# Kernel tuning notes

Hardware: AMD Instinct MI355X
Metric: run time of the kernel (lower is better)

## Reference

```python
import jax, jax.numpy as jnp
import numpy as np

DIM_MODEL = 1024
NUM_HEADS = 16
DROPOUT_P = 0.5
SCALE = float(np.sqrt(DIM_MODEL // NUM_HEADS))  # NOTE: source MULTIPLIES by this (unusual but faithful)
DROP_KEY = jax.random.key(42)


def setup_inputs() -> dict:
    key = jax.random.key(0)
    ks = jax.random.split(key, 9)
    B, LQ, LK, D = 4, 2048, 2048, DIM_MODEL
    s = 1.0 / np.sqrt(D)
    return {
        "query": jax.random.normal(ks[0], (B, LQ, D), jnp.float32),
        "key": jax.random.normal(ks[1], (B, LK, D), jnp.float32),
        "value": jax.random.normal(ks[2], (B, LK, D), jnp.float32),
        "Wq": jax.random.normal(ks[3], (D, D), jnp.float32) * s,
        "bq": jax.random.normal(ks[4], (D,), jnp.float32) * s,
        "Wk": jax.random.normal(ks[5], (D, D), jnp.float32) * s,
        "bk": jax.random.normal(ks[6], (D,), jnp.float32) * s,
        "Wv": jax.random.normal(ks[7], (D, D), jnp.float32) * s,
        "bv": jax.random.normal(ks[8], (D,), jnp.float32) * s,
    }


def reference(query, key, value, Wq, bq, Wk, bk, Wv, bv):
    # Linear projections (W stored as [in, out])
    q = jnp.einsum('bqd,de->bqe', query, Wq) + bq
    k = jnp.einsum('bkd,de->bke', key, Wk) + bk
    v = jnp.einsum('bkd,de->bke', value, Wv) + bv
    # scores scaled by MULTIPLYING sqrt(d_head), per source
    scores = jnp.einsum('bqe,bke->bqk', q, k) * SCALE
    probs = jax.nn.softmax(scores, axis=-1)
    # dropout (train mode, p=0.5), deterministic fixed key for reproducibility
    keep = jax.random.bernoulli(DROP_KEY, 1.0 - DROPOUT_P, probs.shape)
    probs = jnp.where(keep, probs / (1.0 - DROPOUT_P), 0.0)
    return jnp.einsum('bqk,bke->bqe', probs, v)
```

## Files before the change

kernel.cpp:

```cpp
#include <hip/hip_runtime.h>
#include <math.h>

#define BATCH  4
#define LSEQ   2048
#define DMODEL 1024
#define MROWS  (BATCH * LSEQ)
#define SCORE_SCALE 8.0f

#define THREEFRY_PARTITIONABLE 1

typedef __bf16 bf16_t;
typedef bf16_t bf16x8 __attribute__((ext_vector_type(8)));
typedef bf16_t bf16x4 __attribute__((ext_vector_type(4)));
typedef float  f32x4  __attribute__((ext_vector_type(4)));

#define LDSP(p) ((__attribute__((address_space(3))) void*)(p))
#define GLBP(p) ((const __attribute__((address_space(1))) void*)(p))

__device__ __forceinline__ unsigned rotl32(unsigned x, int r) {
    return (x << r) | (x >> (32 - r));
}

__device__ __forceinline__ void threefry2x32(unsigned k0, unsigned k1,
                                             unsigned x0, unsigned x1,
                                             unsigned& o0, unsigned& o1) {
    const unsigned ks0 = k0, ks1 = k1, ks2 = k0 ^ k1 ^ 0x1BD11BDAu;
    x0 += ks0; x1 += ks1;
#define TF_R(r) { x0 += x1; x1 = rotl32(x1, r); x1 ^= x0; }
    TF_R(13) TF_R(15) TF_R(26) TF_R(6)
    x0 += ks1; x1 += ks2 + 1u;
    TF_R(17) TF_R(29) TF_R(16) TF_R(24)
    x0 += ks2; x1 += ks0 + 2u;
    TF_R(13) TF_R(15) TF_R(26) TF_R(6)
    x0 += ks0; x1 += ks1 + 3u;
    TF_R(17) TF_R(29) TF_R(16) TF_R(24)
    x0 += ks1; x1 += ks2 + 4u;
    TF_R(13) TF_R(15) TF_R(26) TF_R(6)
    x0 += ks2; x1 += ks0 + 5u;
#undef TF_R
    o0 = x0; o1 = x1;
}

__device__ __forceinline__ bool dropout_keep(unsigned n) {
    unsigned o0, o1;
#if THREEFRY_PARTITIONABLE
    threefry2x32(0u, 42u, 0u, n, o0, o1);
    unsigned bits = o0 ^ o1;
#else
    const unsigned HALF = (unsigned)(BATCH * LSEQ) * (unsigned)LSEQ / 2u;
    unsigned c0 = (n < HALF) ? n : (n - HALF);
    unsigned c1 = (n < HALF) ? (n + HALF) : n;
    threefry2x32(0u, 42u, c0, c1, o0, o1);
    unsigned bits = (n < HALF) ? o0 : o1;
#endif
    return bits < 0x80000000u;
}

__global__ __launch_bounds__(256)
void split_all(const float* __restrict__ Xq, const float* __restrict__ Xk,
               const float* __restrict__ Xv,
               bf16_t* __restrict__ hi, bf16_t* __restrict__ lo,
               bf16_t* __restrict__ vh, int n) {
    const int y = blockIdx.y;
    const float* X = (y == 0) ? Xq : (y == 1) ? Xk : Xv;
    long long i = (long long)(blockIdx.x * 256 + threadIdx.x) * 4;
    if (i >= n) return;
    float4 v = *(const float4*)(X + i);
    bf16x4 h, l;
    h[0] = (bf16_t)v.x; l[0] = (bf16_t)(v.x - (float)h[0]);
    h[1] = (bf16_t)v.y; l[1] = (bf16_t)(v.y - (float)h[1]);
    h[2] = (bf16_t)v.z; l[2] = (bf16_t)(v.z - (float)h[2]);
    h[3] = (bf16_t)v.w; l[3] = (bf16_t)(v.w - (float)h[3]);
    if (y < 2) {
        *(bf16x4*)(hi + (long long)y * n + i) = h;
        *(bf16x4*)(lo + (long long)y * n + i) = l;
    } else {
        *(bf16x4*)(vh + i) = h;
    }
}

__global__ __launch_bounds__(256)
void split_transpose3(const float* __restrict__ W0, const float* __restrict__ W1,
                      const float* __restrict__ W2,
                      bf16_t* __restrict__ Th01, bf16_t* __restrict__ Tl01,
                      bf16_t* __restrict__ Thv, bf16_t* __restrict__ Tlv,
                      int Kd, int Nd) {
    __shared__ float t[32][33];
    const int z = blockIdx.z;
    const float* W = (z == 0) ? W0 : (z == 1) ? W1 : W2;
    bf16_t* Th = (z == 2) ? Thv : Th01 + (long long)z * Kd * Nd;
    bf16_t* Tl = (z == 2) ? Tlv : Tl01 + (long long)z * Kd * Nd;
    const int bx = blockIdx.x * 32;
    const int by = blockIdx.y * 32;
    const int tx = threadIdx.x & 31, ty = threadIdx.x >> 5;
#pragma unroll
    for (int i = 0; i < 4; ++i)
        t[ty + i * 8][tx] = W[(long long)(by + ty + i * 8) * Nd + bx + tx];
    __syncthreads();
#pragma unroll
    for (int i = 0; i < 4; ++i) {
        float v = t[tx][ty + i * 8];
        long long idx = (long long)(bx + ty + i * 8) * Kd + by + tx;
        bf16_t h = (bf16_t)v;
        Th[idx] = h;
        Tl[idx] = (bf16_t)(v - (float)h);
    }
}

template <int OUT>
__global__ __launch_bounds__(512, 2)
void gemm_pipe(const bf16_t* __restrict__ A, const bf16_t* __restrict__ B,
               const float* __restrict__ bias,
               float* __restrict__ Cf, bf16_t* __restrict__ Ch,
               int M, int N, int K, float scale,
               long long sA, long long sB, long long sC,
               int NYt, int NZ) {
    constexpr int ABUF = 128 * 32;
    constexpr int BUFE = ABUF + 256 * 32;
    __shared__ __align__(16) bf16_t smem[3 * BUFE];

    const int bid = blockIdx.x;
    const int gid = (bid & 7) * 32 + (bid >> 3);
    const int nzy = NZ * NYt;
    const int nx = gid / nzy;
    const int rem = gid - nx * nzy;
    const int zz = rem / NYt;
    const int my = rem - zz * NYt;
    const long long z = zz;
    const int m0 = my * 128, n0 = nx * 256;

    const int tid = threadIdx.x;
    const int lane = tid & 63;
    const int wave = tid >> 6;
    const int quad = lane >> 4;
    const int l16 = lane & 15;
    const int wm = (wave >> 2) * 64;
    const int wn = (wave & 3) * 64;

    const bf16_t* gA = A + z * sA;
    const bf16_t* gB = B + z * sB;

    const int lrow = lane >> 2;
    const int scol = ((lane & 3) ^ ((lrow >> 1) & 3)) * 8;
    const int sw = (l16 >> 1) & 3;

    auto stage_tile = [&](int k0, bf16_t* base) {
        {
            const int row = (wave << 4) + lrow;
            __builtin_amdgcn_global_load_lds(
                GLBP(gA + (long long)(m0 + row) * K + k0 + scol),
                LDSP(base + row * 32), 16, 0, 0);
        }
#pragma unroll
        for (int r = 0; r < 2; ++r) {
            const int row = (r << 7) + (wave << 4) + lrow;
            __builtin_amdgcn_global_load_lds(
                GLBP(gB + (long long)(n0 + row) * K + k0 + scol),
                LDSP(base + ABUF + row * 32), 16, 0, 0);
        }
    };

    f32x4 acc[4][4];
#pragma unroll
    for (int i = 0; i < 4; ++i)
#pragma unroll
        for (int j = 0; j < 4; ++j)
            acc[i][j] = (f32x4){0.f, 0.f, 0.f, 0.f};

    bf16x8 fa0[4], fb0[4], fa1[4], fb1[4];

    const int NIT = K >> 5;

    bf16_t* p0 = smem;
    bf16_t* p1 = smem + BUFE;
    bf16_t* p2 = smem + 2 * BUFE;

    stage_tile(0, p0);
    stage_tile(32, p1);
    stage_tile(64, p2);
    asm volatile("s_waitcnt vmcnt(3)" ::: "memory");
    asm volatile("s_barrier" ::: "memory");
    __builtin_amdgcn_sched_barrier(0);
#pragma unroll
    for (int i = 0; i < 4; ++i) {
        const int ao = (wm + i * 16 + l16) * 32 + (quad ^ sw) * 8;
        fa0[i] = *(const bf16x8*)(p0 + ao);
    }
#pragma unroll
    for (int j = 0; j < 4; ++j) {
        const int bo = ABUF + (wn + j * 16 + l16) * 32 + (quad ^ sw) * 8;
        fb0[j] = *(const bf16x8*)(p0 + bo);
    }

#define PIPE_ITER(T, FAc, FBc, FAn, FBn)                                      \
    {                                                                         \
        const int t_ = (T);                                                   \
        if (t_ + 1 < NIT) {                                                   \
            _Pragma("unroll")                                                 \
            for (int i = 0; i < 4; ++i) {                                     \
                const int ao = (wm + i * 16 + l16) * 32 + (quad ^ sw) * 8;    \
                FAn[i] = *(const bf16x8*)(p1 + ao);                           \
            }                                                                 \
            _Pragma("unroll")                                                 \
            for (int j = 0; j < 4; ++j) {                                     \
                const int bo = ABUF + (wn + j * 16 + l16) * 32 + (quad ^ sw) * 8; \
                FBn[j] = *(const bf16x8*)(p1 + bo);                           \
            }                                                                 \
        }                                                                     \
        if (t_ + 3 < NIT) stage_tile((t_ + 3) << 5, p0);                      \
        __builtin_amdgcn_s_setprio(1);                                        \
        _Pragma("unroll")                                                     \
        for (int i = 0; i < 4; ++i)                                           \
            _Pragma("unroll")                                                 \
            for (int j = 0; j < 4; ++j)                                       \
                acc[i][j] = __builtin_amdgcn_mfma_f32_16x16x32_bf16(          \
                    FAc[i], FBc[j], acc[i][j], 0, 0, 0);                      \
        __builtin_amdgcn_s_setprio(0);                                        \
        if (t_ + 2 < NIT) {                                                   \
            asm volatile("s_waitcnt lgkmcnt(0)" ::: "memory");                \
            if (t_ + 3 < NIT) asm volatile("s_waitcnt vmcnt(3)" ::: "memory");\
            else              asm volatile("s_waitcnt vmcnt(0)" ::: "memory");\
            asm volatile("s_barrier" ::: "memory");                           \
            __builtin_amdgcn_sched_barrier(0);                                \
        }                                                                     \
        { bf16_t* tmp_ = p0; p0 = p1; p1 = p2; p2 = tmp_; }                   \
    }

    for (int tp = 0; tp < NIT; tp += 2) {
        PIPE_ITER(tp,     fa0, fb0, fa1, fb1)
        PIPE_ITER(tp + 1, fa1, fb1, fa0, fb0)
    }
#undef PIPE_ITER

#pragma unroll
    for (int i = 0; i < 4; ++i)
#pragma unroll
        for (int j = 0; j < 4; ++j) {
            const int n = n0 + wn + j * 16 + l16;
#pragma unroll
            for (int r = 0; r < 4; ++r) {
                const int m = m0 + wm + i * 16 + quad * 4 + r;
                const long long idx = z * sC + (long long)m * N + n;
                float v = acc[i][j][r];
                if constexpr (OUT == 0) {
                    Cf[idx] = v * scale;
                } else {
                    Ch[idx] = (bf16_t)(v + bias[m]);
                }
            }
        }
}

template <int OUT>
__global__ __launch_bounds__(512, 2)
void gemm_mfma_8ph(const bf16_t* __restrict__ Ah, const bf16_t* __restrict__ Al,
                   const bf16_t* __restrict__ Bh, const bf16_t* __restrict__ Bl,
                   const float* __restrict__ bias, const float* __restrict__ bias2,
                   float* __restrict__ Cf, bf16_t* __restrict__ Ch,
                   bf16_t* __restrict__ Cl,
                   int M, int N, int K, float scale,
                   long long sA, long long sB, long long sC,
                   int NYt, int NZ) {
    constexpr int TM = 256, TN = 256;
    constexpr int PLANE = 256 * 32;
    constexpr int HB = 4 * PLANE;
    __shared__ __align__(16) bf16_t smem[2 * HB];

    const int bid = blockIdx.x;
    const int gid = (bid & 7) * 32 + (bid >> 3);
    const int nzy = NZ * NYt;
    const int nx = gid / nzy;
    const int rem = gid - nx * nzy;
    const int zz = rem / NYt;
    const int my = rem - zz * NYt;
    const long long z = zz;
    const int m0 = my * TM, n0 = nx * TN;

    const int tid = threadIdx.x;
    const int lane = tid & 63;
    const int wave = tid >> 6;
    const int quad = lane >> 4;
    const int l16 = lane & 15;
    const int wm = (wave >> 2) * 128;
    const int wn = (wave & 3) * 64;

    const bf16_t* gAh = Ah + z * sA;
    const bf16_t* gAl = Al + z * sA;
    const bf16_t* gBh = Bh + z * sB;
    const bf16_t* gBl = Bl + z * sB;

    const int lrow = lane >> 2;
    const int scol = ((lane & 3) ^ ((lrow >> 1) & 3)) * 8;
    const int sw = (l16 >> 1) & 3;

    auto stage_round = [&](int r, int k0, bf16_t* base) {
        if (r < 4) {
            const int row = ((r & 1) << 7) + (wave << 4) + lrow;
            const bf16_t* src = (r >= 2) ? gBl : gBh;
            bf16_t* dst = base + ((r >= 2) ? 3 : 2) * PLANE + row * 32;
            __builtin_amdgcn_global_load_lds(
                GLBP(src + (long long)(n0 + row) * K + k0 + scol), LDSP(dst), 16, 0, 0);
        } else {
            const int p = r - 4;
            const int row = (p << 5) + ((wave & 2) ? 128 : 0) + ((wave & 1) << 4) + lrow;
            const bf16_t* src = (wave >= 4) ? gAl : gAh;
            bf16_t* dst = base + ((wave >= 4) ? 1 : 0) * PLANE + row * 32;
            __builtin_amdgcn_global_load_lds(
                GLBP(src + (long long)(m0 + row) * K + k0 + scol), LDSP(dst), 16, 0, 0);
        }
    };

    f32x4 acc[8][4];
#pragma unroll
    for (int i = 0; i < 8; ++i)
#pragma unroll
        for (int j = 0; j < 4; ++j)
            acc[i][j] = (f32x4){0.f, 0.f, 0.f, 0.f};

    bf16x8 ah[2][2], al[2][2];
    bf16x8 bfh[4], bfl[4];

#pragma unroll
    for (int r = 0; r < 8; ++r) stage_round(r, 0, smem);
    asm volatile("s_waitcnt vmcnt(0)" ::: "memory");
    asm volatile("s_barrier" ::: "memory");
    __builtin_amdgcn_sched_barrier(0);
#pragma unroll
    for (int i = 0; i < 2; ++i) {
        const int ao = (wm + i * 16 + l16) * 32 + (quad ^ sw) * 8;
        ah[0][i] = *(const bf16x8*)(smem + ao);
        al[0][i] = *(const bf16x8*)(smem + PLANE + ao);
    }
#pragma unroll
    for (int j = 0; j < 4; ++j) {
        const int bo = (wn + j * 16 + l16) * 32 + (quad ^ sw) * 8;
        bfh[j] = *(const bf16x8*)(smem + 2 * PLANE + bo);
        bfl[j] = *(const bf16x8*)(smem + 3 * PLANE + bo);
    }

    const int NIT = K >> 5;
    for (int itp = 0; itp < NIT; itp += 2) {
#pragma unroll
        for (int h = 0; h < 2; ++h) {
            const int it = itp + h;
            const bool more = (it + 1) < NIT;
            const int k1 = (it + 1) << 5;
            bf16_t* cur = smem + h * HB;
            bf16_t* nxt = smem + (h ^ 1) * HB;
#pragma unroll
            for (int ph = 0; ph < 4; ++ph) {
                if (ph < 3) {
#pragma unroll
                    for (int i = 0; i < 2; ++i) {
                        const int ao = (wm + ((ph + 1) * 2 + i) * 16 + l16) * 32 + (quad ^ sw) * 8;
                        ah[(ph + 1) & 1][i] = *(const bf16x8*)(cur + ao);
                        al[(ph + 1) & 1][i] = *(const bf16x8*)(cur + PLANE + ao);
                    }
                } else if (more) {
#pragma unroll
                    for (int i = 0; i < 2; ++i) {
                        const int ao = (wm + i * 16 + l16) * 32 + (quad ^ sw) * 8;
                        ah[0][i] = *(const bf16x8*)(nxt + ao);
                        al[0][i] = *(const bf16x8*)(nxt + PLANE + ao);
                    }
                }
                if (more) {
                    if (ph == 0) {
                        stage_round(0, k1, nxt); stage_round(1, k1, nxt);
                        stage_round(2, k1, nxt); stage_round(3, k1, nxt);
                        stage_round(4, k1, nxt);
                    } else if (ph == 1) {
                        stage_round(5, k1, nxt); stage_round(6, k1, nxt);
                        stage_round(7, k1, nxt);
                    }
                }
                __builtin_amdgcn_s_setprio(1);
#pragma unroll
                for (int i = 0; i < 2; ++i)
#pragma unroll
                    for (int j = 0; j < 4; ++j) {
                        f32x4 a = acc[ph * 2 + i][j];
                        a = __builtin_amdgcn_mfma_f32_16x16x32_bf16(ah[ph & 1][i], bfh[j], a, 0, 0, 0);
                        a = __builtin_amdgcn_mfma_f32_16x16x32_bf16(ah[ph & 1][i], bfl[j], a, 0, 0, 0);
                        a = __builtin_amdgcn_mfma_f32_16x16x32_bf16(al[ph & 1][i], bfh[j], a, 0, 0, 0);
                        acc[ph * 2 + i][j] = a;
                    }
                __builtin_amdgcn_s_setprio(0);
                if (ph == 3 && more) {
#pragma unroll
                    for (int j = 0; j < 4; ++j) {
                        const int bo = (wn + j * 16 + l16) * 32 + (quad ^ sw) * 8;
                        bfh[j] = *(const bf16x8*)(nxt + 2 * PLANE + bo);
                        bfl[j] = *(const bf16x8*)(nxt + 3 * PLANE + bo);
                    }
                }
                if (ph == 1) {
                    if (more) asm volatile("s_waitcnt vmcnt(3)" ::: "memory");
                    else      asm volatile("s_waitcnt vmcnt(0)" ::: "memory");
                    asm volatile("s_barrier" ::: "memory");
                    __builtin_amdgcn_sched_barrier(0);
                } else if (ph == 3 && more) {
                    asm volatile("s_waitcnt vmcnt(1)" ::: "memory");
                    asm volatile("s_barrier" ::: "memory");
                    __builtin_amdgcn_sched_barrier(0);
                }
            }
        }
    }

    const float* bz = (z == 1 && bias2) ? bias2 : bias;
#pragma unroll
    for (int i = 0; i < 8; ++i)
#pragma unroll
        for (int j = 0; j < 4; ++j) {
            const int n = n0 + wn + j * 16 + l16;
            float bvn = 0.f;
            if constexpr (OUT != 0) bvn = bz[n];
#pragma unroll
            for (int r = 0; r < 4; ++r) {
                const int m = m0 + wm + i * 16 + quad * 4 + r;
                const long long idx = z * sC + (long long)m * N + n;
                float v = acc[i][j][r];
                if constexpr (OUT == 0) {
                    Cf[idx] = v * scale;
                } else {
                    v += bvn;
                    bf16_t h = (bf16_t)v;
                    Ch[idx] = h;
                    Cl[idx] = (bf16_t)(v - (float)h);
                }
            }
        }
}

__global__ __launch_bounds__(256)
void softmax_dropout(const float* __restrict__ S, bf16_t* __restrict__ P) {
    const unsigned row = blockIdx.x;
    const float* rp = S + (long long)row * LSEQ;
    const int tid = threadIdx.x;

    float v[8];
    *(float4*)(v)     = *(const float4*)(rp + tid * 8);
    *(float4*)(v + 4) = *(const float4*)(rp + tid * 8 + 4);

    float m = v[0];
#pragma unroll
    for (int e = 1; e < 8; ++e) m = fmaxf(m, v[e]);
#pragma unroll
    for (int o = 1; o < 64; o <<= 1) m = fmaxf(m, __shfl_xor(m, o));
    __shared__ float redm[4];
    if ((tid & 63) == 0) redm[tid >> 6] = m;
    __syncthreads();
    m = fmaxf(fmaxf(redm[0], redm[1]), fmaxf(redm[2], redm[3]));

    float s = 0.f;
#pragma unroll
    for (int e = 0; e < 8; ++e) { v[e] = __expf(v[e] - m); s += v[e]; }
#pragma unroll
    for (int o = 1; o < 64; o <<= 1) s += __shfl_xor(s, o);
    __shared__ float reds[4];
    if ((tid & 63) == 0) reds[tid >> 6] = s;
    __syncthreads();
    s = (reds[0] + reds[1]) + (reds[2] + reds[3]);

    const float inv = 2.0f / s;
    const unsigned nb = row * (unsigned)LSEQ + (unsigned)(tid * 8);
    bf16x8 o8;
#pragma unroll
    for (int e = 0; e < 8; ++e)
        o8[e] = (bf16_t)(dropout_keep(nb + e) ? v[e] * inv : 0.0f);
    *(bf16x8*)(P + (long long)row * LSEQ + tid * 8) = o8;
}

extern "C" void kernel_launch(void* const* d_in, const int* in_sizes, int n_in,
                              void* d_out, int out_size, void* d_ws, size_t ws_size,
                              hipStream_t stream) {
    const float* query = (const float*)d_in[0];
    const float* key_  = (const float*)d_in[1];
    const float* value = (const float*)d_in[2];
    const float* Wq = (const float*)d_in[3];
    const float* bq = (const float*)d_in[4];
    const float* Wk = (const float*)d_in[5];
    const float* bk = (const float*)d_in[6];
    const float* Wv = (const float*)d_in[7];
    const float* bv = (const float*)d_in[8];
    float* out = (float*)d_out;

    char* w = (char*)d_ws;
    const size_t Q1 = (size_t)MROWS * DMODEL * 2;
    const long long DD = (long long)DMODEL * DMODEL;
    bf16_t* Qh  = (bf16_t*)(w);
    bf16_t* Ql  = (bf16_t*)(w + 2 * Q1);
    bf16_t* VT  = (bf16_t*)(w + 4 * Q1);
    float*  S   = (float*)(w + 5 * Q1);
    bf16_t* XvH  = (bf16_t*)(w);
    bf16_t* WvTh = (bf16_t*)(w + 2 * Q1);
    bf16_t* WvTl = WvTh + DD;
    bf16_t* XqkH = (bf16_t*)(w + 5 * Q1);
    bf16_t* XqkL = (bf16_t*)(w + 7 * Q1);
    bf16_t* WTh = (bf16_t*)(w + 9 * Q1);
    bf16_t* WTl = (bf16_t*)(w + 9 * Q1 + 2 * (size_t)DMODEL * DMODEL * 2);
    bf16_t* P   = Qh;

    dim3 b256(256);
    dim3 b512(512);
    const int NELEM = MROWS * DMODEL;

    split_transpose3<<<dim3(DMODEL / 32, DMODEL / 32, 3), b256, 0, stream>>>(
        Wq, Wk, Wv, WTh, WTl, WvTh, WvTl, DMODEL, DMODEL);
    split_all<<<dim3(NELEM / 1024, 3), b256, 0, stream>>>(
        query, key_, value, XqkH, XqkL, XvH, NELEM);

    gemm_pipe<2><<<dim3(256), b512, 0, stream>>>(
        WvTh, XvH, bv, nullptr, VT,
        DMODEL, LSEQ, DMODEL, 1.f,
        0, (long long)LSEQ * DMODEL, (long long)DMODEL * LSEQ,
        DMODEL / 128, 4);

    gemm_mfma_8ph<1><<<dim3(256), b512, 0, stream>>>(
        XqkH, XqkL, WTh, WTl, bq, bk, nullptr, Qh, Ql,
        MROWS, DMODEL, DMODEL, 1.f,
        (long long)NELEM, DD, (long long)NELEM,
        MROWS / 256, 2);

    gemm_mfma_8ph<0><<<dim3(256), b512, 0, stream>>>(
        Qh, Ql, Qh + NELEM, Ql + NELEM, nullptr, nullptr, S, nullptr, nullptr,
        LSEQ, LSEQ, DMODEL, SCORE_SCALE,
        (long long)LSEQ * DMODEL, (long long)LSEQ * DMODEL,
        (long long)LSEQ * LSEQ,
        LSEQ / 256, 4);

    softmax_dropout<<<dim3(MROWS), b256, 0, stream>>>(S, P);

    gemm_pipe<0><<<dim3(256), b512, 0, stream>>>(
        P, VT, nullptr, out, nullptr,
        LSEQ, DMODEL, LSEQ, 1.f,
        (long long)LSEQ * LSEQ, (long long)DMODEL * LSEQ, (long long)LSEQ * DMODEL,
        LSEQ / 128, 4);
}
```

Measured before the change: 423.3 us.

## Fuse fp32 hi/lo bf16 split of Q/K inputs into projection GEMM loads

The separate split_all pass over query/key/value is removed. The Q/K projection GEMM now streams fp32 activations directly into LDS and splits them into bf16 hi/lo fragments while reading from LDS, and value gets a plain bf16 conversion kernel. This avoids writing and re-reading the hi/lo bf16 activation buffers in global memory. In exchange, each A fragment costs twice the LDS bytes and extra convert instructions inside the MFMA loop, which could hurt the tight pipeline.

Result: slower. 434.5 us (+2.6%).

```diff
diff --git a/kernel.cpp b/kernel.cpp
--- a/kernel.cpp
+++ b/kernel.cpp
@@ -57,26 +57,15 @@
 }
 
 __global__ __launch_bounds__(256)
-void split_all(const float* __restrict__ Xq, const float* __restrict__ Xk,
-               const float* __restrict__ Xv,
-               bf16_t* __restrict__ hi, bf16_t* __restrict__ lo,
-               bf16_t* __restrict__ vh, int n) {
-    const int y = blockIdx.y;
-    const float* X = (y == 0) ? Xq : (y == 1) ? Xk : Xv;
-    long long i = (long long)(blockIdx.x * 256 + threadIdx.x) * 4;
+void cvt_bf16(const float* __restrict__ X, bf16_t* __restrict__ Y, int n) {
+    long long i = (long long)(blockIdx.x * 256 + threadIdx.x) * 8;
     if (i >= n) return;
-    float4 v = *(const float4*)(X + i);
-    bf16x4 h, l;
-    h[0] = (bf16_t)v.x; l[0] = (bf16_t)(v.x - (float)h[0]);
-    h[1] = (bf16_t)v.y; l[1] = (bf16_t)(v.y - (float)h[1]);
-    h[2] = (bf16_t)v.z; l[2] = (bf16_t)(v.z - (float)h[2]);
-    h[3] = (bf16_t)v.w; l[3] = (bf16_t)(v.w - (float)h[3]);
-    if (y < 2) {
-        *(bf16x4*)(hi + (long long)y * n + i) = h;
-        *(bf16x4*)(lo + (long long)y * n + i) = l;
-    } else {
-        *(bf16x4*)(vh + i) = h;
-    }
+    float4 a = *(const float4*)(X + i);
+    float4 b = *(const float4*)(X + i + 4);
+    bf16x8 o;
+    o[0] = (bf16_t)a.x; o[1] = (bf16_t)a.y; o[2] = (bf16_t)a.z; o[3] = (bf16_t)a.w;
+    o[4] = (bf16_t)b.x; o[5] = (bf16_t)b.y; o[6] = (bf16_t)b.z; o[7] = (bf16_t)b.w;
+    *(bf16x8*)(Y + i) = o;
 }
 
 __global__ __launch_bounds__(256)
@@ -251,9 +240,10 @@
         }
 }
 
-template <int OUT>
+template <int OUT, int ASPLIT>
 __global__ __launch_bounds__(512, 2)
-void gemm_mfma_8ph(const bf16_t* __restrict__ Ah, const bf16_t* __restrict__ Al,
+void gemm_mfma_8ph(const float* __restrict__ Af0, const float* __restrict__ Af1,
+                   const bf16_t* __restrict__ Ah, const bf16_t* __restrict__ Al,
                    const bf16_t* __restrict__ Bh, const bf16_t* __restrict__ Bl,
                    const float* __restrict__ bias, const float* __restrict__ bias2,
                    float* __restrict__ Cf, bf16_t* __restrict__ Ch,
@@ -284,8 +274,9 @@
     const int wm = (wave >> 2) * 128;
     const int wn = (wave & 3) * 64;
 
-    const bf16_t* gAh = Ah + z * sA;
-    const bf16_t* gAl = Al + z * sA;
+    const bf16_t* gAh = ASPLIT ? nullptr : Ah + z * sA;
+    const bf16_t* gAl = ASPLIT ? nullptr : Al + z * sA;
+    const float*  gAf = ASPLIT ? (z ? Af1 : Af0) : nullptr;
     const bf16_t* gBh = Bh + z * sB;
     const bf16_t* gBl = Bl + z * sB;
 
@@ -300,6 +291,16 @@
             bf16_t* dst = base + ((r >= 2) ? 3 : 2) * PLANE + row * 32;
             __builtin_amdgcn_global_load_lds(
                 GLBP(src + (long long)(n0 + row) * K + k0 + scol), LDSP(dst), 16, 0, 0);
+        } else if constexpr (ASPLIT) {
+            const int p = r - 4;
+            const int row = (p << 5) + ((wave & 4) ? 128 : 0)
+                          + ((wave & 3) << 3) + (lane >> 3);
+            const int c = lane & 7;
+            const int kr = (row >> 1) & 3;
+            const int sc = (2 * ((c >> 1) ^ kr) + (c & 1)) * 4;
+            bf16_t* dst = base + row * 64;
+            __builtin_amdgcn_global_load_lds(
+                GLBP(gAf + (long long)(m0 + row) * K + k0 + sc), LDSP(dst), 16, 0, 0);
         } else {
             const int p = r - 4;
             const int row = (p << 5) + ((wave & 2) ? 128 : 0) + ((wave & 1) << 4) + lrow;
@@ -310,6 +311,25 @@
         }
     };
 
+    auto read_afrag = [&](bf16_t* buf, int f, bf16x8& hh, bf16x8& ll) {
+        if constexpr (ASPLIT) {
+            const float* Afp = (const float*)buf;
+            const int row = wm + f * 16 + l16;
+            const float* pp = Afp + row * 32 + ((quad ^ sw) * 8);
+            f32x4 r0 = *(const f32x4*)pp;
+            f32x4 r1 = *(const f32x4*)(pp + 4);
+#pragma unroll
+            for (int e = 0; e < 4; ++e) {
+                hh[e] = (bf16_t)r0[e]; ll[e] = (bf16_t)(r0[e] - (float)hh[e]);
+                hh[4 + e] = (bf16_t)r1[e]; ll[4 + e] = (bf16_t)(r1[e] - (float)hh[4 + e]);
+            }
+        } else {
+            const int ao = (wm + f * 16 + l16) * 32 + (quad ^ sw) * 8;
+            hh = *(const bf16x8*)(buf + ao);
+            ll = *(const bf16x8*)(buf + PLANE + ao);
+        }
+    };
+
     f32x4 acc[8][4];
 #pragma unroll
     for (int i = 0; i < 8; ++i)
@@ -326,11 +346,7 @@
     asm volatile("s_barrier" ::: "memory");
     __builtin_amdgcn_sched_barrier(0);
 #pragma unroll
-    for (int i = 0; i < 2; ++i) {
-        const int ao = (wm + i * 16 + l16) * 32 + (quad ^ sw) * 8;
-        ah[0][i] = *(const bf16x8*)(smem + ao);
-        al[0][i] = *(const bf16x8*)(smem + PLANE + ao);
-    }
+    for (int i = 0; i < 2; ++i) read_afrag(smem, i, ah[0][i], al[0][i]);
 #pragma unroll
     for (int j = 0; j < 4; ++j) {
         const int bo = (wn + j * 16 + l16) * 32 + (quad ^ sw) * 8;
@@ -351,18 +367,12 @@
             for (int ph = 0; ph < 4; ++ph) {
                 if (ph < 3) {
 #pragma unroll
-                    for (int i = 0; i < 2; ++i) {
-                        const int ao = (wm + ((ph + 1) * 2 + i) * 16 + l16) * 32 + (quad ^ sw) * 8;
-                        ah[(ph + 1) & 1][i] = *(const bf16x8*)(cur + ao);
-                        al[(ph + 1) & 1][i] = *(const bf16x8*)(cur + PLANE + ao);
-                    }
+                    for (int i = 0; i < 2; ++i)
+                        read_afrag(cur, (ph + 1) * 2 + i, ah[(ph + 1) & 1][i], al[(ph + 1) & 1][i]);
                 } else if (more) {
 #pragma unroll
-                    for (int i = 0; i < 2; ++i) {
-                        const int ao = (wm + i * 16 + l16) * 32 + (quad ^ sw) * 8;
-                        ah[0][i] = *(const bf16x8*)(nxt + ao);
-                        al[0][i] = *(const bf16x8*)(nxt + PLANE + ao);
-                    }
+                    for (int i = 0; i < 2; ++i)
+                        read_afrag(nxt, i, ah[0][i], al[0][i]);
                 }
                 if (more) {
                     if (ph == 0) {
@@ -496,8 +506,6 @@
     bf16_t* XvH  = (bf16_t*)(w);
     bf16_t* WvTh = (bf16_t*)(w + 2 * Q1);
     bf16_t* WvTl = WvTh + DD;
-    bf16_t* XqkH = (bf16_t*)(w + 5 * Q1);
-    bf16_t* XqkL = (bf16_t*)(w + 7 * Q1);
     bf16_t* WTh = (bf16_t*)(w + 9 * Q1);
     bf16_t* WTl = (bf16_t*)(w + 9 * Q1 + 2 * (size_t)DMODEL * DMODEL * 2);
     bf16_t* P   = Qh;
@@ -508,8 +516,7 @@
 
     split_transpose3<<<dim3(DMODEL / 32, DMODEL / 32, 3), b256, 0, stream>>>(
         Wq, Wk, Wv, WTh, WTl, WvTh, WvTl, DMODEL, DMODEL);
-    split_all<<<dim3(NELEM / 1024, 3), b256, 0, stream>>>(
-        query, key_, value, XqkH, XqkL, XvH, NELEM);
+    cvt_bf16<<<dim3(NELEM / 2048), b256, 0, stream>>>(value, XvH, NELEM);
 
     gemm_pipe<2><<<dim3(256), b512, 0, stream>>>(
         WvTh, XvH, bv, nullptr, VT,
@@ -517,14 +524,15 @@
         0, (long long)LSEQ * DMODEL, (long long)DMODEL * LSEQ,
         DMODEL / 128, 4);
 
-    gemm_mfma_8ph<1><<<dim3(256), b512, 0, stream>>>(
-        XqkH, XqkL, WTh, WTl, bq, bk, nullptr, Qh, Ql,
+    gemm_mfma_8ph<1, 1><<<dim3(256), b512, 0, stream>>>(
+        query, key_, nullptr, nullptr, WTh, WTl, bq, bk, nullptr, Qh, Ql,
         MROWS, DMODEL, DMODEL, 1.f,
-        (long long)NELEM, DD, (long long)NELEM,
+        0, DD, (long long)NELEM,
         MROWS / 256, 2);
 
-    gemm_mfma_8ph<0><<<dim3(256), b512, 0, stream>>>(
-        Qh, Ql, Qh + NELEM, Ql + NELEM, nullptr, nullptr, S, nullptr, nullptr,
+    gemm_mfma_8ph<0, 0><<<dim3(256), b512, 0, stream>>>(
+        nullptr, nullptr, Qh, Ql, Qh + NELEM, Ql + NELEM, nullptr, nullptr,
+        S, nullptr, nullptr,
         LSEQ, LSEQ, DMODEL, SCORE_SCALE,
         (long long)LSEQ * DMODEL, (long long)LSEQ * DMODEL,
         (long long)LSEQ * LSEQ,
```
